# Kernel tuning notes

Hardware: AMD Instinct MI355X
Metric: run time of the kernel (lower is better)

The kernel has to match this reference:

```python
import jax, jax.numpy as jnp
import numpy as np

B, S, D = 8, 4096, 1536
NUM_ORGANISMS = 4
OUT = 2048


def setup_inputs() -> dict:
    key = jax.random.key(0)
    k_x, k_idx, k_w = jax.random.split(key, 3)
    x = jax.random.normal(k_x, (B, S, D), dtype=jnp.float32)
    organism_index = jax.random.randint(k_idx, (B,), 0, NUM_ORGANISMS, dtype=jnp.int32)
    # TruncatedNormal(stddev=1/sqrt(D)) init; plain normal*stddev is a faithful stand-in
    stddev = 1.0 / np.sqrt(D)
    w = jax.random.normal(k_w, (NUM_ORGANISMS, D, OUT), dtype=jnp.float32) * stddev
    b = jnp.zeros((NUM_ORGANISMS, OUT), dtype=jnp.float32)
    return {"x": x, "organism_index": organism_index, "w": w, "b": b}


def reference(x, organism_index, w, b):
    # Gather per-batch organism weights/biases (hard routing), then batched matmul.
    w_b = w[organism_index]          # [B, D, OUT]
    b_b = b[organism_index]          # [B, OUT]
    out = jnp.einsum('bsi,bij->bsj', x, w_b,
                     preferred_element_type=jnp.float32)  # [B, S, OUT]
    return out + b_b[:, None, :]
```

## Files before the change

kernel.cpp:

```cpp
#include <hip/hip_runtime.h>
#include <hip/hip_bf16.h>
#include <stdint.h>

#define B_    8
#define S_    4096
#define D_    1536
#define ORG_  4
#define OUT_  2048

typedef __bf16 bf16;
typedef __attribute__((ext_vector_type(8)))  bf16  bf16x8;
typedef __attribute__((ext_vector_type(4)))  float f32x4;
typedef __attribute__((ext_vector_type(16))) float f32x16;

#define BK64 64
#define NKT  (D_ / BK64)

__global__ void k_cvt_x(const float* __restrict__ x, bf16* __restrict__ xb, long n8) {
  long i = (long)blockIdx.x * blockDim.x + threadIdx.x;
  long stride = (long)gridDim.x * blockDim.x;
  for (; i < n8; i += stride) {
    const float4* p = (const float4*)(x + i * 8);
    float4 a = p[0];
    float4 b = p[1];
    bf16x8 v;
    v[0] = (bf16)a.x; v[1] = (bf16)a.y; v[2] = (bf16)a.z; v[3] = (bf16)a.w;
    v[4] = (bf16)b.x; v[5] = (bf16)b.y; v[6] = (bf16)b.z; v[7] = (bf16)b.w;
    *(bf16x8*)(xb + i * 8) = v;
  }
}

__global__ void k_cvt_wT(const float* __restrict__ w, bf16* __restrict__ wt) {
  __shared__ float tile[32][33];
  int org = blockIdx.z;
  int n0 = blockIdx.x * 32;
  int d0 = blockIdx.y * 32;
  const float* wsrc = w + (size_t)org * D_ * OUT_;
  bf16* wdst = wt + (size_t)org * OUT_ * D_;
  int tx = threadIdx.x, ty = threadIdx.y;
#pragma unroll
  for (int j = 0; j < 32; j += 8)
    tile[ty + j][tx] = wsrc[(size_t)(d0 + ty + j) * OUT_ + (n0 + tx)];
  __syncthreads();
#pragma unroll
  for (int j = 0; j < 32; j += 8)
    wdst[(size_t)(n0 + ty + j) * D_ + (d0 + tx)] = (bf16)tile[tx][ty + j];
}

__global__ __launch_bounds__(512, 2)
void k_gemm256(const bf16* __restrict__ xb, const bf16* __restrict__ wt,
               const int* __restrict__ oidx, const float* __restrict__ bias,
               float* __restrict__ out) {
  __shared__ __align__(16) char smem[131072];
  char* const ldsA = smem;
  char* const ldsB = smem + 65536;

  const int batch = blockIdx.y;
  const int bx = blockIdx.x;
  const int swz = (bx & 7) * 16 + (bx >> 3);
  const int tn = swz >> 4, tm = swz & 15;
  const int m0 = tm * 256, n0 = tn * 256;
  const int org = oidx[batch];

  const bf16* Ag = xb + (size_t)batch * S_ * D_ + (size_t)m0 * D_;
  const bf16* Bg = wt + (size_t)org * OUT_ * D_ + (size_t)n0 * D_;

  const int tid  = threadIdx.x;
  const int lane = tid & 63, wv = tid >> 6;
  const int wr = wv >> 2, wc = wv & 3;
  const int l31 = lane & 31, hi = lane >> 5;

  const int xorv = ((lane & 7) ^ ((lane >> 3) & 3)) << 4;
  const int off[4] = { (0  + hi * 16) ^ xorv, (32 + hi * 16) ^ xorv,
                       (64 + hi * 16) ^ xorv, (96 + hi * 16) ^ xorv };
  const int arow = (wr * 128 + l31) * 128;
  const int brow = (wc * 64  + l31) * 128;

  const int srow = tid >> 3;
  const int scol = (((tid & 7) ^ ((tid >> 3) & 7) ^ ((tid >> 6) & 3))) << 3;
  const int soff = wv * 1024;

#define LDA(v, mt, ks) (*(const bf16x8*)(ldsA + (v)*32768 + arow + (mt)*4096 + off[ks]))
#define LDB(v, nt, ks) (*(const bf16x8*)(ldsB + (v)*32768 + brow + (nt)*4096 + off[ks]))

#define STAGE_HALF(gptr, ldsbase, h, kb) do {                                            \
    __builtin_amdgcn_global_load_lds(                                                    \
      (__attribute__((address_space(1))) void*)((gptr) + (size_t)((h)*128 + srow) * D_ + (kb) + scol), \
      (__attribute__((address_space(3))) void*)((ldsbase) + (h)*16384 + soff), 16, 0, 0);\
    __builtin_amdgcn_global_load_lds(                                                    \
      (__attribute__((address_space(1))) void*)((gptr) + (size_t)((h)*128 + 64 + srow) * D_ + (kb) + scol), \
      (__attribute__((address_space(3))) void*)((ldsbase) + (h)*16384 + 8192 + soff), 16, 0, 0); \
  } while (0)

#define SBAR()  __builtin_amdgcn_s_barrier()
#define LGK0()  asm volatile("s_waitcnt lgkmcnt(0)" ::: "memory")
#define VMC4()  asm volatile("s_waitcnt vmcnt(4)" ::: "memory")
#define VMC0()  asm volatile("s_waitcnt vmcnt(0)" ::: "memory")
#define PRIO(p) __builtin_amdgcn_s_setprio(p)

  bf16x8 a[2][4], b0[4], b1[4];
  f32x16 acc[4][2];
#pragma unroll
  for (int mt = 0; mt < 4; ++mt)
#pragma unroll
    for (int nt = 0; nt < 2; ++nt)
#pragma unroll
      for (int rr = 0; rr < 16; ++rr) acc[mt][nt][rr] = 0.f;

#define READ_A2(v, mbase) do { _Pragma("unroll") for (int mm = 0; mm < 2; ++mm) \
    _Pragma("unroll") for (int ks = 0; ks < 4; ++ks) \
      a[mm][ks] = LDA(v, (mbase) + mm, ks); } while (0)
#define READ_B4(v, nt, bb) do { _Pragma("unroll") for (int ks = 0; ks < 4; ++ks) \
      bb[ks] = LDB(v, nt, ks); } while (0)
#define MFMA_O(mbase, nt, bb) do { \
    _Pragma("unroll") for (int mm = 0; mm < 2; ++mm) \
    _Pragma("unroll") for (int ks = 0; ks < 4; ++ks) \
      acc[(mbase)+mm][nt] = __builtin_amdgcn_mfma_f32_32x32x16_bf16( \
          a[mm][ks], bb[ks], acc[(mbase)+mm][nt], 0, 0, 0); } while (0)

  STAGE_HALF(Bg, ldsB, 0, 0);
  STAGE_HALF(Bg, ldsB, 1, 0);
  STAGE_HALF(Ag, ldsA, 0, 0);
  STAGE_HALF(Ag, ldsA, 1, 0);
  STAGE_HALF(Bg, ldsB + 32768, 0, BK64);
  STAGE_HALF(Bg, ldsB + 32768, 1, BK64);
  VMC4();
  SBAR();

  for (int i = 0; i < NKT / 2; ++i) {
    const int k1 = (2 * i + 1) * BK64;
    int t2 = 2 * i + 2; if (t2 > NKT - 1) t2 = NKT - 1;
    int t3 = 2 * i + 3; if (t3 > NKT - 1) t3 = NKT - 1;
    const int k2 = t2 * BK64, k3 = t3 * BK64;

    READ_A2(0, 0); READ_B4(0, 0, b0);
    STAGE_HALF(Ag, ldsA + 32768, 0, k1);
    SBAR(); LGK0();
    PRIO(1); MFMA_O(0, 0, b0); PRIO(0);
    SBAR();
    READ_B4(0, 1, b1);
    STAGE_HALF(Ag, ldsA + 32768, 1, k1);
    SBAR(); LGK0();
    PRIO(1); MFMA_O(0, 1, b1); PRIO(0);
    SBAR();
    READ_A2(0, 2);
    STAGE_HALF(Bg, ldsB, 0, k2);
    SBAR(); LGK0();
    PRIO(1); MFMA_O(2, 0, b0); PRIO(0);
    SBAR();
    STAGE_HALF(Bg, ldsB, 1, k2);
    SBAR();
    PRIO(1); MFMA_O(2, 1, b1); PRIO(0);
    VMC4();
    SBAR();
    READ_A2(1, 0); READ_B4(1, 0, b0);
    STAGE_HALF(Ag, ldsA, 0, k2);
    SBAR(); LGK0();
    PRIO(1); MFMA_O(0, 0, b0); PRIO(0);
    SBAR();
    READ_B4(1, 1, b1);
    STAGE_HALF(Ag, ldsA, 1, k2);
    SBAR(); LGK0();
    PRIO(1); MFMA_O(0, 1, b1); PRIO(0);
    SBAR();
    READ_A2(1, 2);
    STAGE_HALF(Bg, ldsB + 32768, 0, k3);
    SBAR(); LGK0();
    PRIO(1); MFMA_O(2, 0, b0); PRIO(0);
    SBAR();
    STAGE_HALF(Bg, ldsB + 32768, 1, k3);
    SBAR();
    PRIO(1); MFMA_O(2, 1, b1); PRIO(0);
    VMC4();
    SBAR();
  }

  VMC0();

  float* Og = out + (size_t)batch * S_ * OUT_ + (size_t)m0 * OUT_ + n0;
  const float* bbase = bias + (size_t)org * OUT_ + n0;
#pragma unroll
  for (int nt = 0; nt < 2; ++nt) {
    const int col = wc * 64 + nt * 32 + l31;
    const float bv = bbase[col];
#pragma unroll
    for (int mt = 0; mt < 4; ++mt) {
#pragma unroll
      for (int rr = 0; rr < 16; ++rr) {
        const int row = wr * 128 + mt * 32 + 4 * hi + (rr & 3) + 8 * (rr >> 2);
        Og[(size_t)row * OUT_ + col] = acc[mt][nt][rr] + bv;
      }
    }
  }
#undef LDA
#undef LDB
#undef STAGE_HALF
#undef SBAR
#undef LGK0
#undef VMC4
#undef VMC0
#undef PRIO
#undef READ_A2
#undef READ_B4
#undef MFMA_O
}

__global__ void k_gemm_fallback(const float* __restrict__ x, const int* __restrict__ oidx,
                                const float* __restrict__ w, const float* __restrict__ bias,
                                float* __restrict__ out) {
  const int b = blockIdx.z;
  const int org = oidx[b];
  const int n = blockIdx.x * 64 + threadIdx.x;
  const int m = blockIdx.y * 4 + threadIdx.y;
  const float* xr = x + ((size_t)b * S_ + m) * D_;
  const float* wp = w + (size_t)org * D_ * OUT_ + n;
  float acc = 0.f;
  for (int k = 0; k < D_; ++k) acc += xr[k] * wp[(size_t)k * OUT_];
  out[((size_t)b * S_ + m) * OUT_ + n] = acc + bias[(size_t)org * OUT_ + n];
}

extern "C" void kernel_launch(void* const* d_in, const int* in_sizes, int n_in,
                              void* d_out, int out_size, void* d_ws, size_t ws_size,
                              hipStream_t stream) {
  const float* x    = (const float*)d_in[0];
  const int*   oidx = (const int*)d_in[1];
  const float* w    = (const float*)d_in[2];
  const float* bias = (const float*)d_in[3];
  float* out = (float*)d_out;

  const size_t xb_elems = (size_t)B_ * S_ * D_;
  const size_t wt_elems = (size_t)ORG_ * OUT_ * D_;
  const size_t need = (xb_elems + wt_elems) * sizeof(bf16);

  if (ws_size < need) {
    dim3 g(OUT_ / 64, S_ / 4, B_);
    k_gemm_fallback<<<g, dim3(64, 4), 0, stream>>>(x, oidx, w, bias, out);
    return;
  }

  bf16* xb = (bf16*)d_ws;
  bf16* wt = xb + xb_elems;

  k_cvt_x<<<2048, 256, 0, stream>>>(x, xb, (long)(xb_elems / 8));
  dim3 gt(OUT_ / 32, D_ / 32, ORG_);
  k_cvt_wT<<<gt, dim3(32, 8), 0, stream>>>(w, wt);
  dim3 gg(128, B_);
  k_gemm256<<<gg, 512, 0, stream>>>(xb, wt, oidx, bias, out);
}
```

Measured before the change: 305.2 us.

## Fuse fp32-to-bf16 conversion of x into GEMM A-tile staging

Removes the separate x conversion kernel and its bf16 workspace round trip. The GEMM now loads fp32 A tiles into registers, converts them to bf16 and writes them into swizzled LDS, instead of copying pre-converted data with direct global-to-LDS loads. This avoids writing and rereading about 100 MB of converted activations. The cost is that each GEMM block reads twice as many bytes for A, uses more registers, and issues extra LDS writes and conversion instructions inside the pipelined loop, and A is reread by all 8 column tiles.

After: 430.1 us. 1.41x slower.

```diff
diff --git a/kernel.cpp b/kernel.cpp
--- a/kernel.cpp
+++ b/kernel.cpp
@@ -10,25 +10,10 @@
 
 typedef __bf16 bf16;
 typedef __attribute__((ext_vector_type(8)))  bf16  bf16x8;
-typedef __attribute__((ext_vector_type(4)))  float f32x4;
 typedef __attribute__((ext_vector_type(16))) float f32x16;
 
 #define BK64 64
 #define NKT  (D_ / BK64)
-
-__global__ void k_cvt_x(const float* __restrict__ x, bf16* __restrict__ xb, long n8) {
-  long i = (long)blockIdx.x * blockDim.x + threadIdx.x;
-  long stride = (long)gridDim.x * blockDim.x;
-  for (; i < n8; i += stride) {
-    const float4* p = (const float4*)(x + i * 8);
-    float4 a = p[0];
-    float4 b = p[1];
-    bf16x8 v;
-    v[0] = (bf16)a.x; v[1] = (bf16)a.y; v[2] = (bf16)a.z; v[3] = (bf16)a.w;
-    v[4] = (bf16)b.x; v[5] = (bf16)b.y; v[6] = (bf16)b.z; v[7] = (bf16)b.w;
-    *(bf16x8*)(xb + i * 8) = v;
-  }
-}
 
 __global__ void k_cvt_wT(const float* __restrict__ w, bf16* __restrict__ wt) {
   __shared__ float tile[32][33];
@@ -48,7 +33,7 @@
 }
 
 __global__ __launch_bounds__(512, 2)
-void k_gemm256(const bf16* __restrict__ xb, const bf16* __restrict__ wt,
+void k_gemm256(const float* __restrict__ x, const bf16* __restrict__ wt,
                const int* __restrict__ oidx, const float* __restrict__ bias,
                float* __restrict__ out) {
   __shared__ __align__(16) char smem[131072];
@@ -62,8 +47,8 @@
   const int m0 = tm * 256, n0 = tn * 256;
   const int org = oidx[batch];
 
-  const bf16* Ag = xb + (size_t)batch * S_ * D_ + (size_t)m0 * D_;
-  const bf16* Bg = wt + (size_t)org * OUT_ * D_ + (size_t)n0 * D_;
+  const float* Af = x  + (size_t)batch * S_ * D_ + (size_t)m0 * D_;
+  const bf16*  Bg = wt + (size_t)org * OUT_ * D_ + (size_t)n0 * D_;
 
   const int tid  = threadIdx.x;
   const int lane = tid & 63, wv = tid >> 6;
@@ -80,16 +65,44 @@
   const int scol = (((tid & 7) ^ ((tid >> 3) & 7) ^ ((tid >> 6) & 3))) << 3;
   const int soff = wv * 1024;
 
+  const int s_arow = tid >> 2;
+  const int cb0    = (tid & 3) * 2;
+  const int s_acol = cb0 * 8;
+  const int akey   = (s_arow & 7) ^ ((s_arow >> 3) & 3);
+
 #define LDA(v, mt, ks) (*(const bf16x8*)(ldsA + (v)*32768 + arow + (mt)*4096 + off[ks]))
 #define LDB(v, nt, ks) (*(const bf16x8*)(ldsB + (v)*32768 + brow + (nt)*4096 + off[ks]))
 
-#define STAGE_HALF(gptr, ldsbase, h, kb) do {                                            \
+#define STAGE_B(h, kb, vbase) do {                                                       \
     __builtin_amdgcn_global_load_lds(                                                    \
-      (__attribute__((address_space(1))) void*)((gptr) + (size_t)((h)*128 + srow) * D_ + (kb) + scol), \
-      (__attribute__((address_space(3))) void*)((ldsbase) + (h)*16384 + soff), 16, 0, 0);\
+      (__attribute__((address_space(1))) void*)(Bg + (size_t)((h)*128 + srow) * D_ + (kb) + scol), \
+      (__attribute__((address_space(3))) void*)((vbase) + (h)*16384 + soff), 16, 0, 0);  \
     __builtin_amdgcn_global_load_lds(                                                    \
-      (__attribute__((address_space(1))) void*)((gptr) + (size_t)((h)*128 + 64 + srow) * D_ + (kb) + scol), \
-      (__attribute__((address_space(3))) void*)((ldsbase) + (h)*16384 + 8192 + soff), 16, 0, 0); \
+      (__attribute__((address_space(1))) void*)(Bg + (size_t)((h)*128 + 64 + srow) * D_ + (kb) + scol), \
+      (__attribute__((address_space(3))) void*)((vbase) + (h)*16384 + 8192 + soff), 16, 0, 0); \
+  } while (0)
+
+#define A_LOAD(la, h, kb) do {                                                           \
+    const float* s_ = Af + (size_t)((h)*128 + s_arow) * D_ + (kb) + s_acol;              \
+    la[0] = *(const float4*)(s_);      la[1] = *(const float4*)(s_ + 4);                 \
+    la[2] = *(const float4*)(s_ + 8);  la[3] = *(const float4*)(s_ + 12);                \
+  } while (0)
+
+#define CVT8(dst, f0, f1) do {                                                           \
+    dst[0]=(bf16)(f0).x; dst[1]=(bf16)(f0).y; dst[2]=(bf16)(f0).z; dst[3]=(bf16)(f0).w;  \
+    dst[4]=(bf16)(f1).x; dst[5]=(bf16)(f1).y; dst[6]=(bf16)(f1).z; dst[7]=(bf16)(f1).w;  \
+  } while (0)
+
+#define WRITE_A2(vbase) do {                                                             \
+    bf16x8 v_;                                                                           \
+    CVT8(v_, la0[0], la0[1]);                                                            \
+    *(bf16x8*)((vbase) + s_arow*128 + ((cb0 ^ akey) << 4)) = v_;                         \
+    CVT8(v_, la0[2], la0[3]);                                                            \
+    *(bf16x8*)((vbase) + s_arow*128 + (((cb0 + 1) ^ akey) << 4)) = v_;                   \
+    CVT8(v_, la1[0], la1[1]);                                                            \
+    *(bf16x8*)((vbase) + 16384 + s_arow*128 + ((cb0 ^ akey) << 4)) = v_;                 \
+    CVT8(v_, la1[2], la1[3]);                                                            \
+    *(bf16x8*)((vbase) + 16384 + s_arow*128 + (((cb0 + 1) ^ akey) << 4)) = v_;           \
   } while (0)
 
 #define SBAR()  __builtin_amdgcn_s_barrier()
@@ -98,6 +111,7 @@
 #define VMC0()  asm volatile("s_waitcnt vmcnt(0)" ::: "memory")
 #define PRIO(p) __builtin_amdgcn_s_setprio(p)
 
+  float4 la0[4], la1[4];
   bf16x8 a[2][4], b0[4], b1[4];
   f32x16 acc[4][2];
 #pragma unroll
@@ -118,13 +132,15 @@
       acc[(mbase)+mm][nt] = __builtin_amdgcn_mfma_f32_32x32x16_bf16( \
           a[mm][ks], bb[ks], acc[(mbase)+mm][nt], 0, 0, 0); } while (0)
 
-  STAGE_HALF(Bg, ldsB, 0, 0);
-  STAGE_HALF(Bg, ldsB, 1, 0);
-  STAGE_HALF(Ag, ldsA, 0, 0);
-  STAGE_HALF(Ag, ldsA, 1, 0);
-  STAGE_HALF(Bg, ldsB + 32768, 0, BK64);
-  STAGE_HALF(Bg, ldsB + 32768, 1, BK64);
+  STAGE_B(0, 0, ldsB);
+  STAGE_B(1, 0, ldsB);
+  A_LOAD(la0, 0, 0);
+  A_LOAD(la1, 1, 0);
+  STAGE_B(0, BK64, ldsB + 32768);
+  STAGE_B(1, BK64, ldsB + 32768);
   VMC4();
+  WRITE_A2(ldsA);
+  LGK0();
   SBAR();
 
   for (int i = 0; i < NKT / 2; ++i) {
@@ -134,44 +150,48 @@
     const int k2 = t2 * BK64, k3 = t3 * BK64;
 
     READ_A2(0, 0); READ_B4(0, 0, b0);
-    STAGE_HALF(Ag, ldsA + 32768, 0, k1);
+    A_LOAD(la0, 0, k1);
     SBAR(); LGK0();
     PRIO(1); MFMA_O(0, 0, b0); PRIO(0);
     SBAR();
     READ_B4(0, 1, b1);
-    STAGE_HALF(Ag, ldsA + 32768, 1, k1);
+    A_LOAD(la1, 1, k1);
     SBAR(); LGK0();
     PRIO(1); MFMA_O(0, 1, b1); PRIO(0);
     SBAR();
     READ_A2(0, 2);
-    STAGE_HALF(Bg, ldsB, 0, k2);
+    STAGE_B(0, k2, ldsB);
     SBAR(); LGK0();
     PRIO(1); MFMA_O(2, 0, b0); PRIO(0);
     SBAR();
-    STAGE_HALF(Bg, ldsB, 1, k2);
-    SBAR();
+    STAGE_B(1, k2, ldsB);
+    SBAR();
+    VMC4();
+    WRITE_A2(ldsA + 32768);
     PRIO(1); MFMA_O(2, 1, b1); PRIO(0);
+    LGK0();
+    SBAR();
+    READ_A2(1, 0); READ_B4(1, 0, b0);
+    A_LOAD(la0, 0, k2);
+    SBAR(); LGK0();
+    PRIO(1); MFMA_O(0, 0, b0); PRIO(0);
+    SBAR();
+    READ_B4(1, 1, b1);
+    A_LOAD(la1, 1, k2);
+    SBAR(); LGK0();
+    PRIO(1); MFMA_O(0, 1, b1); PRIO(0);
+    SBAR();
+    READ_A2(1, 2);
+    STAGE_B(0, k3, ldsB + 32768);
+    SBAR(); LGK0();
+    PRIO(1); MFMA_O(2, 0, b0); PRIO(0);
+    SBAR();
+    STAGE_B(1, k3, ldsB + 32768);
+    SBAR();
     VMC4();
-    SBAR();
-    READ_A2(1, 0); READ_B4(1, 0, b0);
-    STAGE_HALF(Ag, ldsA, 0, k2);
-    SBAR(); LGK0();
-    PRIO(1); MFMA_O(0, 0, b0); PRIO(0);
-    SBAR();
-    READ_B4(1, 1, b1);
-    STAGE_HALF(Ag, ldsA, 1, k2);
-    SBAR(); LGK0();
-    PRIO(1); MFMA_O(0, 1, b1); PRIO(0);
-    SBAR();
-    READ_A2(1, 2);
-    STAGE_HALF(Bg, ldsB + 32768, 0, k3);
-    SBAR(); LGK0();
-    PRIO(1); MFMA_O(2, 0, b0); PRIO(0);
-    SBAR();
-    STAGE_HALF(Bg, ldsB + 32768, 1, k3);
-    SBAR();
+    WRITE_A2(ldsA);
     PRIO(1); MFMA_O(2, 1, b1); PRIO(0);
-    VMC4();
+    LGK0();
     SBAR();
   }
 
@@ -194,7 +214,10 @@
   }
 #undef LDA
 #undef LDB
-#undef STAGE_HALF
+#undef STAGE_B
+#undef A_LOAD
+#undef CVT8
+#undef WRITE_A2
 #undef SBAR
 #undef LGK0
 #undef VMC4
@@ -228,9 +251,8 @@
   const float* bias = (const float*)d_in[3];
   float* out = (float*)d_out;
 
-  const size_t xb_elems = (size_t)B_ * S_ * D_;
   const size_t wt_elems = (size_t)ORG_ * OUT_ * D_;
-  const size_t need = (xb_elems + wt_elems) * sizeof(bf16);
+  const size_t need = wt_elems * sizeof(bf16);
 
   if (ws_size < need) {
     dim3 g(OUT_ / 64, S_ / 4, B_);
@@ -238,12 +260,10 @@
     return;
   }
 
-  bf16* xb = (bf16*)d_ws;
-  bf16* wt = xb + xb_elems;
-
-  k_cvt_x<<<2048, 256, 0, stream>>>(x, xb, (long)(xb_elems / 8));
+  bf16* wt = (bf16*)d_ws;
+
   dim3 gt(OUT_ / 32, D_ / 32, ORG_);
   k_cvt_wT<<<gt, dim3(32, 8), 0, stream>>>(w, wt);
   dim3 gg(128, B_);
-  k_gemm256<<<gg, 512, 0, stream>>>(xb, wt, oidx, bias, out);
-}
+  k_gemm256<<<gg, 512, 0, stream>>>(x, wt, oidx, bias, out);
+}
```
